# Performance work log

Measured on AMD Instinct MI355X. Metric: run time of the kernel, lower is better.

## Reference

```python
import jax, jax.numpy as jnp
import numpy as np
import math

B, T, C = 1, 2048, 2048
NH, HS = 16, 128          # hs = C // nh
NLQ, NLKV, DHR = 1536, 512, 64


def _rope(x, cos, sin):
    # x: [B, T, H, D]; cos/sin: [T, D//2]. Rotates pairs (even, odd) like
    # torch's complex-multiply apply_rotary_emb.
    xr = x.reshape(x.shape[:-1] + (-1, 2))
    x_re, x_im = xr[..., 0], xr[..., 1]
    c = cos[None, :, None, :]
    s = sin[None, :, None, :]
    out = jnp.stack([x_re * c - x_im * s, x_re * s + x_im * c], axis=-1)
    return out.reshape(x.shape)


def setup_inputs() -> dict:
    key = jax.random.key(0)
    ks = jax.random.split(key, 9)
    sc = 0.02  # init scale so logits stay sane
    x = jax.random.normal(ks[0], (B, T, C), jnp.float32)
    # RoPE tables (theta = 10000), matching precompute_freqs_cis
    inv = 1.0 / (10000.0 ** (jnp.arange(0, DHR, 2, dtype=jnp.float32) / DHR))
    ang = jnp.outer(jnp.arange(T, dtype=jnp.float32), inv)  # [T, DHR//2]
    return {
        "x": x,
        "freqs_cos": jnp.cos(ang),
        "freqs_sin": jnp.sin(ang),
        "W_dq": jax.random.normal(ks[1], (NLQ, C), jnp.float32) * sc,
        "W_uq": jax.random.normal(ks[2], (C, NLQ), jnp.float32) * sc,
        "W_dkv": jax.random.normal(ks[3], (NLKV, C), jnp.float32) * sc,
        "W_uk": jax.random.normal(ks[4], (C, NLKV), jnp.float32) * sc,
        "W_uv": jax.random.normal(ks[5], (C, NLKV), jnp.float32) * sc,
        "W_qr": jax.random.normal(ks[6], (NH * DHR, NLQ), jnp.float32) * sc,
        "W_kr": jax.random.normal(ks[7], (DHR, C), jnp.float32) * sc,
        "W_o": jax.random.normal(ks[8], (C, C), jnp.float32) * sc,
    }


def reference(x, freqs_cos, freqs_sin, W_dq, W_uq, W_dkv, W_uk, W_uv, W_qr, W_kr, W_o):
    # ---- low-rank query/kv down-projections ----
    c_q = x @ W_dq.T                       # [B,T,NLQ]
    c_kv = x @ W_dkv.T                     # [B,T,NLKV]  (no kv_cache: c_kv = new_c_kv)

    # ---- weight absorption (training path) ----
    # torch: W_uq.weight.view(1,nlq,nh,hs).transpose(1,2) @ W_uk.weight.view(1,nh,hs,nlkv)
    Wuq_h = W_uq.reshape(NLQ, NH, HS).transpose(1, 0, 2)   # [NH,NLQ,HS]
    Wuk_h = W_uk.reshape(NH, HS, NLKV)                     # [NH,HS,NLKV]
    k_eff = jnp.einsum('hql,hlk->hqk', Wuq_h, Wuk_h)       # [NH,NLQ,NLKV]
    # torch: (W_uv.weight.T @ W_o.weight.T).view(nlkv,nh,hs).transpose(0,1)
    v_eff = (W_uv.T @ W_o.T).reshape(NLKV, NH, HS).transpose(1, 0, 2)  # [NH,NLKV,HS]

    # ---- content attention scores in latent space ----
    attn_c = jnp.einsum('bhtk,bsk->bhts',
                        jnp.einsum('btq,hqk->bhtk', c_q, k_eff), c_kv)  # [B,NH,T,T]

    # ---- decoupled RoPE subspace ----
    k_r = _rope((x @ W_kr.T)[:, :, None, :], freqs_cos, freqs_sin)[:, :, 0, :]   # [B,T,DHR]
    q_r = _rope((c_q @ W_qr.T).reshape(B, T, NH, DHR), freqs_cos, freqs_sin)
    q_r = q_r.transpose(0, 2, 1, 3)                                              # [B,NH,T,DHR]
    attn_r = jnp.einsum('bhtd,bsd->bhts', q_r, k_r)                              # [B,NH,T,T]

    # ---- combine, causal mask, softmax ----
    scale = 1.0 / math.sqrt(HS + DHR)
    scores = (attn_c + attn_r) * scale
    causal = jnp.tril(jnp.ones((T, T), dtype=bool))  # mask = triu(diag=1) complement
    scores = jnp.where(causal[None, None], scores, jnp.float32(-jnp.inf))
    attn = jax.nn.softmax(scores, axis=-1)           # dropout p=0.0

    # ---- value path: attend in latent space, then absorbed up+output proj ----
    y_lat = jnp.einsum('bhts,bsk->bhtk', attn, c_kv)          # [B,NH,T,NLKV]
    y = jnp.einsum('bhtk,hkd->bhtd', y_lat, v_eff)            # [B,NH,T,HS]
    y = y.transpose(0, 2, 1, 3).reshape(B, T, C)              # [B,T,C] (W_o absorbed)
    return y
```

## Files before the change

kernel.cpp:

```cpp
#include <hip/hip_runtime.h>
#include <hip/hip_bf16.h>
#include <math.h>

typedef __bf16 bf16_t;
typedef __bf16 bf16x4 __attribute__((ext_vector_type(4)));
typedef __bf16 bf16x8 __attribute__((ext_vector_type(8)));
typedef float f32x4 __attribute__((ext_vector_type(4)));

#define T_DIM 2048
#define C_DIM 2048
#define NH 16
#define HS 128
#define NLQ 1536
#define NLKV 512
#define DHR 64
#define QKD 192

__device__ __forceinline__ int probe_f32(const bf16_t* __restrict__ x) {
  int lane = threadIdx.x & 63;
  int bad = 0;
#pragma unroll
  for (int i = 0; i < 4; ++i) {
    float v = (float)x[lane + i * 64];
    if (!(fabsf(v) < 1.0e6f)) bad = 1;
  }
  return (__ballot(bad) != 0ull) ? 1 : 0;
}

struct PrepPack {
  const void* src[9];
  bf16_t* dst[9];
  int n[9];
  const void* tsrc[2];
  bf16_t* tdst[2];
  int tR[2], tC[2], tbx[2];
};

__global__ __launch_bounds__(256) void prep_k(PrepPack p, const bf16_t* __restrict__ xprobe) {
  __shared__ bf16_t tile[32][33];
  const int f32 = probe_f32(xprobe);
  const int which = blockIdx.y;
  if (which < 9) {
    const int n = p.n[which];
    const int stride = gridDim.x * 256 * 8;
    for (int i = (blockIdx.x * 256 + threadIdx.x) * 8; i < n; i += stride) {
      if (f32) {
        const float* s = (const float*)p.src[which] + i;
        f32x4 lo = *(const f32x4*)s;
        f32x4 hi = *(const f32x4*)(s + 4);
        bf16x8 v;
#pragma unroll
        for (int j = 0; j < 4; ++j) { v[j] = (bf16_t)lo[j]; v[j + 4] = (bf16_t)hi[j]; }
        *(bf16x8*)(p.dst[which] + i) = v;
      } else {
        *(bf16x8*)(p.dst[which] + i) = *(const bf16x8*)((const bf16_t*)p.src[which] + i);
      }
    }
  } else {
    const int ts = which - 9;
    const int R = p.tR[ts], C = p.tC[ts], tbx = p.tbx[ts];
    const int ntiles = tbx * (R / 32);
    if ((int)blockIdx.x >= ntiles) return;
    const void* in = p.tsrc[ts];
    bf16_t* out = p.tdst[ts];
    int bx = (blockIdx.x % tbx) * 32, by = (blockIdx.x / tbx) * 32;
    int tx = threadIdx.x & 31, ty = threadIdx.x >> 5;
    for (int i = ty; i < 32; i += 8) {
      int r = by + i, c = bx + tx;
      size_t idx = (size_t)r * C + c;
      tile[i][tx] = f32 ? (bf16_t)((const float*)in)[idx] : ((const bf16_t*)in)[idx];
    }
    __syncthreads();
    for (int i = ty; i < 32; i += 8) {
      int r = bx + i, c = by + tx;
      out[(size_t)r * R + c] = tile[tx][i];
    }
  }
}

__device__ __forceinline__ void async16(const bf16_t* g, bf16_t* l) {
  __builtin_amdgcn_global_load_lds(
      (const __attribute__((address_space(1))) void*)g,
      (__attribute__((address_space(3))) void*)l, 16, 0, 0);
}

#define BM 128
#define BN 128

struct GDesc {
  const bf16_t* A; const bf16_t* B; bf16_t* C;
  int M, N, K, lda, ldb, ldc, mb, bx0;
};
struct GGrp { GDesc d[3]; };

__global__ __launch_bounds__(256) void gemm_group(GGrp g, int nseg) {
  int bx = blockIdx.x;
  int s = 0;
  while (s + 1 < nseg && bx >= g.d[s + 1].bx0) ++s;
  const GDesc D = g.d[s];
  const int local = bx - D.bx0;
  const int bm = (local % D.mb) * BM, bn = (local / D.mb) * BN;

  __shared__ bf16_t As[BM * 32];
  __shared__ bf16_t Bs[BN * 32];
  const int tid = threadIdx.x;
  const int lane = tid & 63;
  const int wave = tid >> 6;
  const int l16 = lane & 15, quad = lane >> 4;
  const int wm = (wave >> 1) * 64, wn = (wave & 1) * 64;
  const int srow = lane >> 2;
  const int scol = (lane & 3) * 8;
  f32x4 acc[4][4] = {};

  for (int k0 = 0; k0 < D.K; k0 += 32) {
    __syncthreads();
#pragma unroll
    for (int pss = 0; pss < 2; ++pss) {
      int rowT = pss * 64 + wave * 16 + srow;
      int ar = bm + rowT; if (ar > D.M - 1) ar = D.M - 1;
      async16(D.A + (size_t)ar * D.lda + k0 + scol, As + (pss * 64 + wave * 16) * 32);
      int br = bn + rowT; if (br > D.N - 1) br = D.N - 1;
      async16(D.B + (size_t)br * D.ldb + k0 + scol, Bs + (pss * 64 + wave * 16) * 32);
    }
    __syncthreads();
    bf16x8 af[4], bfr[4];
#pragma unroll
    for (int i = 0; i < 4; ++i)
      af[i] = *(const bf16x8*)(As + (wm + i * 16 + l16) * 32 + quad * 8);
#pragma unroll
    for (int j = 0; j < 4; ++j)
      bfr[j] = *(const bf16x8*)(Bs + (wn + j * 16 + l16) * 32 + quad * 8);
#pragma unroll
    for (int i = 0; i < 4; ++i)
#pragma unroll
      for (int j = 0; j < 4; ++j)
        acc[i][j] = __builtin_amdgcn_mfma_f32_16x16x32_bf16(af[i], bfr[j], acc[i][j], 0, 0, 0);
  }
#pragma unroll
  for (int i = 0; i < 4; ++i)
#pragma unroll
    for (int j = 0; j < 4; ++j)
#pragma unroll
      for (int r = 0; r < 4; ++r) {
        int gm = bm + wm + i * 16 + quad * 4 + r;
        int gn = bn + wn + j * 16 + l16;
        if (gm < D.M && gn < D.N) D.C[(size_t)gm * D.ldc + gn] = (bf16_t)acc[i][j][r];
      }
}

__global__ void pack_qk_k(const bf16_t* __restrict__ qcat, const bf16_t* __restrict__ khead,
                          const bf16_t* __restrict__ xa,
                          const bf16_t* __restrict__ fc, const bf16_t* __restrict__ fs,
                          bf16_t* __restrict__ Qp, bf16_t* __restrict__ Kp) {
  int idx = blockIdx.x * blockDim.x + threadIdx.x;
  if (idx >= NH * T_DIM * 96) return;
  int j = idx % 96;
  int t = (idx / 96) % T_DIM;
  int h = idx / (96 * T_DIM);
  if (blockIdx.y == 0) {
    const float scale = 0.07216878364870323f;
    bf16_t* out = Qp + ((size_t)h * T_DIM + t) * QKD;
    if (j < 64) {
      float a = (float)qcat[(size_t)t * 3072 + h * HS + 2 * j];
      float b = (float)qcat[(size_t)t * 3072 + h * HS + 2 * j + 1];
      out[2 * j] = (bf16_t)(a * scale);
      out[2 * j + 1] = (bf16_t)(b * scale);
    } else {
      int i = j - 64;
      float re = (float)qcat[(size_t)t * 3072 + 2048 + h * DHR + 2 * i];
      float im = (float)qcat[(size_t)t * 3072 + 2048 + h * DHR + 2 * i + 1];
      float c = (float)fc[t * 32 + i], s = (float)fs[t * 32 + i];
      out[HS + 2 * i] = (bf16_t)((re * c - im * s) * scale);
      out[HS + 2 * i + 1] = (bf16_t)((re * s + im * c) * scale);
    }
  } else {
    bf16_t* out = Kp + ((size_t)h * T_DIM + t) * QKD;
    if (j < 64) {
      out[2 * j] = khead[(size_t)t * C_DIM + h * HS + 2 * j];
      out[2 * j + 1] = khead[(size_t)t * C_DIM + h * HS + 2 * j + 1];
    } else {
      int i = j - 64;
      float re = (float)xa[(size_t)t * 2112 + 2048 + 2 * i];
      float im = (float)xa[(size_t)t * 2112 + 2048 + 2 * i + 1];
      float c = (float)fc[t * 32 + i], s = (float)fs[t * 32 + i];
      out[HS + 2 * i] = (bf16_t)(re * c - im * s);
      out[HS + 2 * i + 1] = (bf16_t)(re * s + im * c);
    }
  }
}

#define FBM 128
#define FBN 64
#define KPITCH 200
#define VPITCH 72
#define PPITCH 72

__global__ __launch_bounds__(256) void flash_k(const bf16_t* __restrict__ Qp,
                                               const bf16_t* __restrict__ Kp,
                                               const bf16_t* __restrict__ VT,
                                               void* __restrict__ Y,
                                               const bf16_t* __restrict__ xprobe,
                                               float* __restrict__ Opart,
                                               float* __restrict__ Mpart,
                                               float* __restrict__ Lpart) {
  __shared__ bf16_t Ksm[FBN * KPITCH];
  __shared__ bf16_t Vtsm[HS * VPITCH];
  __shared__ bf16_t Psm[4][32 * PPITCH];
  const int tid = threadIdx.x;
  const int lane = tid & 63, wave = tid >> 6;
  const int l16 = lane & 15, quad = lane >> 4;
  const int id = blockIdx.x;
  const int xcd = id & 7, slot = id >> 3;
  const int h = xcd + 8 * (slot / 24);
  const int p = slot % 24;
  int qt, kt0, kt1, partial;
  if (p < 16) {
    qt = 8 + (p >> 1);
    int half = qt + 1;
    kt0 = (p & 1) ? half : 0;
    kt1 = (p & 1) ? (2 * qt + 2) : half;
    partial = 1;
  } else {
    qt = 23 - p; kt0 = 0; kt1 = 2 * qt + 2; partial = 0;
  }
  const int qb = qt * FBM;
  const int f32out = probe_f32(xprobe);

  bf16x8 aq[2][6];
#pragma unroll
  for (int tt = 0; tt < 2; ++tt) {
    const bf16_t* qbase = Qp + ((size_t)h * T_DIM + qb + wave * 32 + tt * 16 + l16) * QKD;
#pragma unroll
    for (int c = 0; c < 6; ++c) aq[tt][c] = *(const bf16x8*)(qbase + c * 32 + quad * 8);
  }

  f32x4 o[2][8] = {};
  float m_i[2] = {-3.0e38f, -3.0e38f}, l_i[2] = {0.f, 0.f};

  const bf16_t* kg_base = Kp + (size_t)h * T_DIM * QKD;
  const bf16_t* vg_base = VT + (size_t)(h * HS) * T_DIM;

  bf16x8 kreg[6], vreg[4];
  {
    const bf16_t* kg = kg_base + (size_t)kt0 * FBN * QKD;
#pragma unroll
    for (int i = 0; i < 6; ++i) {
      int idx = i * 256 + tid;
      kreg[i] = *(const bf16x8*)(kg + (size_t)idx * 8);
    }
    const bf16_t* vg = vg_base + kt0 * FBN;
#pragma unroll
    for (int i = 0; i < 4; ++i) {
      int idx = i * 256 + tid, row = idx >> 3, c8 = idx & 7;
      vreg[i] = *(const bf16x8*)(vg + (size_t)row * T_DIM + c8 * 8);
    }
  }

  for (int kt = kt0; kt < kt1; ++kt) {
    __syncthreads();
#pragma unroll
    for (int i = 0; i < 6; ++i) {
      int idx = i * 256 + tid, row = idx / 24, c8 = idx % 24;
      *(bf16x8*)(Ksm + row * KPITCH + c8 * 8) = kreg[i];
    }
#pragma unroll
    for (int i = 0; i < 4; ++i) {
      int idx = i * 256 + tid, row = idx >> 3, c8 = idx & 7;
      *(bf16x8*)(Vtsm + row * VPITCH + c8 * 8) = vreg[i];
    }
    __syncthreads();
    if (kt + 1 < kt1) {
      const bf16_t* kg = kg_base + (size_t)(kt + 1) * FBN * QKD;
#pragma unroll
      for (int i = 0; i < 6; ++i) {
        int idx = i * 256 + tid;
        kreg[i] = *(const bf16x8*)(kg + (size_t)idx * 8);
      }
      const bf16_t* vg = vg_base + (kt + 1) * FBN;
#pragma unroll
      for (int i = 0; i < 4; ++i) {
        int idx = i * 256 + tid, row = idx >> 3, c8 = idx & 7;
        vreg[i] = *(const bf16x8*)(vg + (size_t)row * T_DIM + c8 * 8);
      }
    }
    f32x4 sc[2][4] = {};
#pragma unroll
    for (int nt = 0; nt < 4; ++nt)
#pragma unroll
      for (int c = 0; c < 6; ++c) {
        bf16x8 bk = *(const bf16x8*)(Ksm + (nt * 16 + l16) * KPITCH + c * 32 + quad * 8);
        sc[0][nt] = __builtin_amdgcn_mfma_f32_16x16x32_bf16(bk, aq[0][c], sc[0][nt], 0, 0, 0);
        sc[1][nt] = __builtin_amdgcn_mfma_f32_16x16x32_bf16(bk, aq[1][c], sc[1][nt], 0, 0, 0);
      }
    if (kt >= 2 * qt) {
#pragma unroll
      for (int tt = 0; tt < 2; ++tt) {
        int t_glob = qb + wave * 32 + tt * 16 + l16;
#pragma unroll
        for (int nt = 0; nt < 4; ++nt) {
          int s_base = kt * FBN + nt * 16 + quad * 4;
#pragma unroll
          for (int r = 0; r < 4; ++r)
            if (s_base + r > t_glob) sc[tt][nt][r] = -3.0e38f;
        }
      }
    }
#pragma unroll
    for (int tt = 0; tt < 2; ++tt) {
      float mx = sc[tt][0][0];
#pragma unroll
      for (int nt = 0; nt < 4; ++nt)
#pragma unroll
        for (int r = 0; r < 4; ++r) mx = fmaxf(mx, sc[tt][nt][r]);
      mx = fmaxf(mx, __shfl_xor(mx, 16, 64));
      mx = fmaxf(mx, __shfl_xor(mx, 32, 64));
      float mn = fmaxf(m_i[tt], mx);
      float alpha = exp2f((m_i[tt] - mn) * 1.4426950408889634f);
      float rs = 0.f;
#pragma unroll
      for (int nt = 0; nt < 4; ++nt) {
        bf16x4 pk;
#pragma unroll
        for (int r = 0; r < 4; ++r) {
          float pv = exp2f((sc[tt][nt][r] - mn) * 1.4426950408889634f);
          rs += pv;
          pk[r] = (bf16_t)pv;
        }
        *(bf16x4*)(&Psm[wave][(tt * 16 + l16) * PPITCH + nt * 16 + quad * 4]) = pk;
      }
      rs += __shfl_xor(rs, 16, 64);
      rs += __shfl_xor(rs, 32, 64);
      l_i[tt] = l_i[tt] * alpha + rs;
      m_i[tt] = mn;
#pragma unroll
      for (int dt = 0; dt < 8; ++dt) o[tt][dt] *= alpha;
    }
#pragma unroll
    for (int s2 = 0; s2 < 2; ++s2) {
      bf16x8 ap0 = *(const bf16x8*)(&Psm[wave][l16 * PPITCH + s2 * 32 + quad * 8]);
      bf16x8 ap1 = *(const bf16x8*)(&Psm[wave][(16 + l16) * PPITCH + s2 * 32 + quad * 8]);
#pragma unroll
      for (int dt = 0; dt < 8; ++dt) {
        bf16x8 bv = *(const bf16x8*)(Vtsm + (dt * 16 + l16) * VPITCH + s2 * 32 + quad * 8);
        o[0][dt] = __builtin_amdgcn_mfma_f32_16x16x32_bf16(bv, ap0, o[0][dt], 0, 0, 0);
        o[1][dt] = __builtin_amdgcn_mfma_f32_16x16x32_bf16(bv, ap1, o[1][dt], 0, 0, 0);
      }
    }
  }

  if (!partial) {
#pragma unroll
    for (int tt = 0; tt < 2; ++tt) {
      float inv = 1.0f / l_i[tt];
      int t = qb + wave * 32 + tt * 16 + l16;
#pragma unroll
      for (int dt = 0; dt < 8; ++dt) {
        size_t oi = (size_t)t * C_DIM + h * HS + dt * 16 + quad * 4;
        if (f32out) {
          f32x4 v;
#pragma unroll
          for (int r = 0; r < 4; ++r) v[r] = o[tt][dt][r] * inv;
          *(f32x4*)((float*)Y + oi) = v;
        } else {
          bf16x4 v;
#pragma unroll
          for (int r = 0; r < 4; ++r) v[r] = (bf16_t)(o[tt][dt][r] * inv);
          *(bf16x4*)((bf16_t*)Y + oi) = v;
        }
      }
    }
  } else {
    const int pi = h * 16 + p;
#pragma unroll
    for (int tt = 0; tt < 2; ++tt) {
      int rowl = wave * 32 + tt * 16 + l16;
      float* ob = Opart + ((size_t)pi * 128 + rowl) * 128;
#pragma unroll
      for (int dt = 0; dt < 8; ++dt) {
        f32x4 v = o[tt][dt];
        *(f32x4*)(ob + dt * 16 + quad * 4) = v;
      }
      if (quad == 0) {
        Mpart[(size_t)pi * 128 + rowl] = m_i[tt];
        Lpart[(size_t)pi * 128 + rowl] = l_i[tt];
      }
    }
  }
}

__global__ __launch_bounds__(256) void combine_k(const float* __restrict__ Opart,
                                                 const float* __restrict__ Mpart,
                                                 const float* __restrict__ Lpart,
                                                 void* __restrict__ Y,
                                                 const bf16_t* __restrict__ xprobe) {
  const int h = blockIdx.y;
  const int qi = blockIdx.x;
  const int pi0 = h * 16 + qi * 2, pi1 = pi0 + 1;
  const int row = threadIdx.x >> 1;
  const int c0 = (threadIdx.x & 1) * 64;
  const int f32out = probe_f32(xprobe);
  float m0 = Mpart[(size_t)pi0 * 128 + row], m1 = Mpart[(size_t)pi1 * 128 + row];
  float l0 = Lpart[(size_t)pi0 * 128 + row], l1 = Lpart[(size_t)pi1 * 128 + row];
  float ms = fmaxf(m0, m1);
  float w0 = exp2f((m0 - ms) * 1.4426950408889634f);
  float w1 = exp2f((m1 - ms) * 1.4426950408889634f);
  float inv = 1.0f / (l0 * w0 + l1 * w1);
  const float* O0 = Opart + ((size_t)pi0 * 128 + row) * 128 + c0;
  const float* O1 = Opart + ((size_t)pi1 * 128 + row) * 128 + c0;
  int t = (8 + qi) * 128 + row;
  size_t ob = (size_t)t * C_DIM + h * HS + c0;
#pragma unroll
  for (int d4 = 0; d4 < 64; d4 += 4) {
    f32x4 a = *(const f32x4*)(O0 + d4);
    f32x4 b = *(const f32x4*)(O1 + d4);
#pragma unroll
    for (int j = 0; j < 4; ++j) {
      float v = (a[j] * w0 + b[j] * w1) * inv;
      if (f32out) ((float*)Y)[ob + d4 + j] = v;
      else        ((bf16_t*)Y)[ob + d4 + j] = (bf16_t)v;
    }
  }
}

extern "C" void kernel_launch(void* const* d_in, const int* in_sizes, int n_in,
                              void* d_out, int out_size, void* d_ws, size_t ws_size,
                              hipStream_t stream) {
  bf16_t* w = (bf16_t*)d_ws;
  const bf16_t* xprobe = (const bf16_t*)d_in[0];

  if (ws_size < (size_t)34472000 * 2 + 128) return;

  bf16_t* fcc    = w + 64;
  bf16_t* fsc    = w + 65600;
  bf16_t* xc     = w + 131136;
  bf16_t* BigB   = w + 4325440;
  bf16_t* dqc    = BigB;
  bf16_t* dkvc   = BigB + 3145728;
  bf16_t* krc    = BigB + 4194304;
  bf16_t* Bq     = w + 8650816;
  bf16_t* W_uq_t = Bq;
  bf16_t* qrc    = Bq + 3145728;
  bf16_t* xa     = w + 13369408;
  bf16_t* qcat   = w + 17694784;
  bf16_t* k_head = w + 23986240;
  bf16_t* vhatT  = w + 28180544;
  bf16_t* ukc    = w + 32374848;
  bf16_t* Pt     = w + 33423424;
  bf16_t* woc    = qcat;
  bf16_t* W_uv_t = k_head;
  bf16_t* Qpack  = xc;
  bf16_t* Kpack  = qcat;
  float* Opart = (float*)(w + 6422592);
  float* Mpart = (float*)(w + 14811200);
  float* Lpart = (float*)(w + 14876736);

  PrepPack pp;
  const void* srcs[9] = {d_in[1], d_in[2], d_in[0], d_in[3], d_in[5], d_in[9], d_in[8], d_in[6], d_in[10]};
  bf16_t* dsts[9]     = {fcc,     fsc,     xc,      dqc,     dkvc,    krc,     qrc,     ukc,     woc};
  int ns[9] = {T_DIM * 32, T_DIM * 32, T_DIM * C_DIM, NLQ * C_DIM, NLKV * C_DIM,
               DHR * C_DIM, NH * DHR * NLQ, C_DIM * NLKV, C_DIM * C_DIM};
  for (int i = 0; i < 9; ++i) { pp.src[i] = srcs[i]; pp.dst[i] = dsts[i]; pp.n[i] = ns[i]; }
  pp.tsrc[0] = d_in[4]; pp.tdst[0] = W_uq_t; pp.tR[0] = 1536; pp.tC[0] = 2048; pp.tbx[0] = 64;
  pp.tsrc[1] = d_in[7]; pp.tdst[1] = W_uv_t; pp.tR[1] = 2048; pp.tC[1] = 512;  pp.tbx[1] = 16;
  prep_k<<<dim3(3072, 11), 256, 0, stream>>>(pp, xprobe);

  {
    GGrp g;
    g.d[0] = {xc,  BigB,   xa, 2048, 2112, 2048, 2048, 2048, 2112, 16, 0};
    g.d[1] = {woc, W_uv_t, Pt, 2048,  512, 2048, 2048, 2048,  512, 16, 272};
    gemm_group<<<336, 256, 0, stream>>>(g, 2);
  }
  {
    GGrp g;
    g.d[0] = {xa,        Bq,        qcat,   2048, 3072, 1536, 2112, 1536, 3072, 16, 0};
    g.d[1] = {xa + 1536, ukc,       k_head, 2048, 2048,  512, 2112,  512, 2048, 16, 384};
    g.d[2] = {Pt,        xa + 1536, vhatT,  2048, 2048,  512,  512, 2112, 2048, 16, 640};
    gemm_group<<<896, 256, 0, stream>>>(g, 3);
  }

  int pk = (NH * T_DIM * 96 + 255) / 256;
  pack_qk_k<<<dim3(pk, 2), 256, 0, stream>>>(qcat, k_head, xa, fcc, fsc, Qpack, Kpack);

  flash_k<<<dim3(384), 256, 0, stream>>>(Qpack, Kpack, vhatT, d_out, xprobe, Opart, Mpart, Lpart);
  combine_k<<<dim3(8, NH), 256, 0, stream>>>(Opart, Mpart, Lpart, d_out, xprobe);
}
```

Measured before the change: 352.6 us.

## Double-buffer grouped GEMM with BK=64 and XOR-swizzled LDS tiles

The grouped GEMM now uses two LDS buffers per operand with a K-tile of 64, issuing async global-to-LDS loads for the next tile while MFMAs run on the current one. LDS columns are XOR-swizzled by row to avoid bank conflicts on fragment reads. It also drops one barrier per iteration. This doubles LDS use to 64KB per block, which may reduce occupancy, and it assumes K is a multiple of 64.

```diff
diff --git a/kernel.cpp b/kernel.cpp
--- a/kernel.cpp
+++ b/kernel.cpp
@@ -86,6 +86,7 @@
 
 #define BM 128
 #define BN 128
+#define BKG 64
 
 struct GDesc {
   const bf16_t* A; const bf16_t* B; bf16_t* C;
@@ -101,41 +102,68 @@
   const int local = bx - D.bx0;
   const int bm = (local % D.mb) * BM, bn = (local / D.mb) * BN;
 
-  __shared__ bf16_t As[BM * 32];
-  __shared__ bf16_t Bs[BN * 32];
+  __shared__ bf16_t As[2][BM * BKG];
+  __shared__ bf16_t Bs[2][BN * BKG];
   const int tid = threadIdx.x;
   const int lane = tid & 63;
   const int wave = tid >> 6;
   const int l16 = lane & 15, quad = lane >> 4;
   const int wm = (wave >> 1) * 64, wn = (wave & 1) * 64;
-  const int srow = lane >> 2;
-  const int scol = (lane & 3) * 8;
   f32x4 acc[4][4] = {};
 
-  for (int k0 = 0; k0 < D.K; k0 += 32) {
-    __syncthreads();
-#pragma unroll
-    for (int pss = 0; pss < 2; ++pss) {
-      int rowT = pss * 64 + wave * 16 + srow;
-      int ar = bm + rowT; if (ar > D.M - 1) ar = D.M - 1;
-      async16(D.A + (size_t)ar * D.lda + k0 + scol, As + (pss * 64 + wave * 16) * 32);
-      int br = bn + rowT; if (br > D.N - 1) br = D.N - 1;
-      async16(D.B + (size_t)br * D.ldb + k0 + scol, Bs + (pss * 64 + wave * 16) * 32);
-    }
-    __syncthreads();
-    bf16x8 af[4], bfr[4];
-#pragma unroll
-    for (int i = 0; i < 4; ++i)
-      af[i] = *(const bf16x8*)(As + (wm + i * 16 + l16) * 32 + quad * 8);
-#pragma unroll
-    for (int j = 0; j < 4; ++j)
-      bfr[j] = *(const bf16x8*)(Bs + (wn + j * 16 + l16) * 32 + quad * 8);
-#pragma unroll
-    for (int i = 0; i < 4; ++i)
-#pragma unroll
-      for (int j = 0; j < 4; ++j)
-        acc[i][j] = __builtin_amdgcn_mfma_f32_16x16x32_bf16(af[i], bfr[j], acc[i][j], 0, 0, 0);
-  }
+  const int nt = D.K / BKG;
+
+#pragma unroll
+  for (int r = 0; r < 4; ++r) {
+    int c = r * 256 + tid;
+    int row = c >> 3;
+    int c8 = (c & 7) ^ (row & 7);
+    int ar = bm + row; if (ar > D.M - 1) ar = D.M - 1;
+    int br = bn + row; if (br > D.N - 1) br = D.N - 1;
+    async16(D.A + (size_t)ar * D.lda + c8 * 8, &As[0][c * 8]);
+    async16(D.B + (size_t)br * D.ldb + c8 * 8, &Bs[0][c * 8]);
+  }
+  asm volatile("s_waitcnt vmcnt(0)" ::: "memory");
+  __builtin_amdgcn_s_barrier();
+
+  for (int t = 0; t < nt; ++t) {
+    const int cur = t & 1;
+    if (t + 1 < nt) {
+      const int k0 = (t + 1) * BKG;
+#pragma unroll
+      for (int r = 0; r < 4; ++r) {
+        int c = r * 256 + tid;
+        int row = c >> 3;
+        int c8 = (c & 7) ^ (row & 7);
+        int ar = bm + row; if (ar > D.M - 1) ar = D.M - 1;
+        int br = bn + row; if (br > D.N - 1) br = D.N - 1;
+        async16(D.A + (size_t)ar * D.lda + k0 + c8 * 8, &As[cur ^ 1][c * 8]);
+        async16(D.B + (size_t)br * D.ldb + k0 + c8 * 8, &Bs[cur ^ 1][c * 8]);
+      }
+    }
+#pragma unroll
+    for (int kk = 0; kk < 2; ++kk) {
+      bf16x8 af[4], bfr[4];
+#pragma unroll
+      for (int i = 0; i < 4; ++i) {
+        int row = wm + i * 16 + l16;
+        af[i] = *(const bf16x8*)(&As[cur][row * BKG + (((kk * 4 + quad) ^ (row & 7)) * 8)]);
+      }
+#pragma unroll
+      for (int j = 0; j < 4; ++j) {
+        int row = wn + j * 16 + l16;
+        bfr[j] = *(const bf16x8*)(&Bs[cur][row * BKG + (((kk * 4 + quad) ^ (row & 7)) * 8)]);
+      }
+#pragma unroll
+      for (int i = 0; i < 4; ++i)
+#pragma unroll
+        for (int j = 0; j < 4; ++j)
+          acc[i][j] = __builtin_amdgcn_mfma_f32_16x16x32_bf16(af[i], bfr[j], acc[i][j], 0, 0, 0);
+    }
+    asm volatile("s_waitcnt vmcnt(0)" ::: "memory");
+    __builtin_amdgcn_s_barrier();
+  }
+
 #pragma unroll
   for (int i = 0; i < 4; ++i)
 #pragma unroll
```

Result: faster. 331.4 us (-6.0%).
